# Optimization experiments

Measured on AMD Instinct MI355X. Metric: run time of the kernel, lower is better.

## Reference

```python
import math
import jax, jax.numpy as jnp
import numpy as np

B, L, D = 2, 2048, 1024
NH = 16
HS = D // NH
BLOCK_SIZE = 2048


def setup_inputs() -> dict:
    key = jax.random.key(0)
    ks = jax.random.split(key, 4)
    x = jax.random.normal(ks[0], (B, L, D), dtype=jnp.float32)
    Wqkv = jax.random.normal(ks[1], (D, 3 * D), dtype=jnp.float32) * 0.02
    bqkv = jnp.zeros((3 * D,), dtype=jnp.float32)
    Wproj = jax.random.normal(ks[2], (D, D), dtype=jnp.float32) * 0.02
    bproj = jnp.zeros((D,), dtype=jnp.float32)
    Er = jax.random.normal(ks[3], (BLOCK_SIZE, HS), dtype=jnp.float32)
    return {"x": x, "Wqkv": Wqkv, "bqkv": bqkv, "Wproj": Wproj, "bproj": bproj, "Er": Er}


def _skew(QEr):
    # QEr: [B, nh, L, L]  (Music Transformer skew trick)
    b, nh, nr, nc = QEr.shape
    padded = jnp.pad(QEr, ((0, 0), (0, 0), (0, 0), (1, 0)))  # [B, nh, nr, nc+1]
    reshaped = padded.reshape(b, nh, nc + 1, nr)
    return reshaped[:, :, 1:, :]  # [B, nh, nr, nc]


def reference(x, Wqkv, bqkv, Wproj, bproj, Er):
    b, l, d = x.shape
    qkv = x @ Wqkv + bqkv  # [B, L, 3D]
    q, k, v = jnp.split(qkv, 3, axis=2)
    q = q.reshape(b, l, NH, HS).transpose(0, 2, 1, 3)  # [B, nh, L, hs]
    k = k.reshape(b, l, NH, HS).transpose(0, 2, 1, 3)
    v = v.reshape(b, l, NH, HS).transpose(0, 2, 1, 3)

    start = BLOCK_SIZE - l
    Er_t = Er[start:, :].T  # [hs, L]
    QEr = jnp.einsum('bhld,dm->bhlm', q, Er_t)  # [B, nh, L, L]
    Srel = _skew(QEr)

    QK_t = jnp.einsum('bhld,bhmd->bhlm', q, k)
    scale = 1.0 / math.sqrt(HS)
    att = (QK_t + Srel) * scale
    causal = jnp.tril(jnp.ones((l, l), dtype=bool))
    att = jnp.where(causal[None, None, :, :], att, jnp.float32(-jnp.inf))
    att = jax.nn.softmax(att, axis=-1)
    y = jnp.einsum('bhlm,bhmd->bhld', att, v)
    y = y.transpose(0, 2, 1, 3).reshape(b, l, d)
    return y @ Wproj + bproj
```

## Files before the change

kernel.cpp:

```cpp
#include <hip/hip_runtime.h>
#include <stdint.h>

#define BB 2
#define LL 2048
#define DD 1024
#define NHH 16
#define HSS 64

typedef __bf16 bf16x8 __attribute__((ext_vector_type(8)));
typedef float f32x4 __attribute__((ext_vector_type(4)));

__device__ __forceinline__ bf16x8 load8(const float* p) {
  float4 f0 = *(const float4*)p;
  float4 f1 = *(const float4*)(p + 4);
  bf16x8 v;
  v[0] = (__bf16)f0.x; v[1] = (__bf16)f0.y; v[2] = (__bf16)f0.z; v[3] = (__bf16)f0.w;
  v[4] = (__bf16)f1.x; v[5] = (__bf16)f1.y; v[6] = (__bf16)f1.z; v[7] = (__bf16)f1.w;
  return v;
}
__device__ __forceinline__ bf16x8 load8(const __bf16* p) {
  return *(const bf16x8*)p;
}

__device__ __forceinline__ void async_ld16(__bf16* lds_uniform_base,
                                           const __bf16* gptr_per_lane) {
  __builtin_amdgcn_global_load_lds(
      (const __attribute__((address_space(1))) void*)gptr_per_lane,
      (__attribute__((address_space(3))) void*)lds_uniform_base, 16, 0, 0);
}

__global__ void prep_k(const float* __restrict__ Wqkv, const float* __restrict__ x,
                       const float* __restrict__ Er, __bf16* __restrict__ WqkvT,
                       __bf16* __restrict__ xb, __bf16* __restrict__ Erb) {
  int tx = threadIdx.x, ty = threadIdx.y;
  int tid = ty * 32 + tx;
  if (blockIdx.z == 1) {
    if (blockIdx.x >= 2048) return;
    size_t off = ((size_t)blockIdx.x * 256 + tid) * 8;
    *(bf16x8*)&xb[off] = load8(&x[off]);
    return;
  }
  if (blockIdx.z == 2) {
    if (blockIdx.x >= 64) return;
    size_t off = ((size_t)blockIdx.x * 256 + tid) * 8;
    *(bf16x8*)&Erb[off] = load8(&Er[off]);
    return;
  }
  __shared__ __bf16 tile[32][33];
  int c0 = (blockIdx.x % 96) * 32, r0 = (blockIdx.x / 96) * 32;
#pragma unroll
  for (int i = ty; i < 32; i += 8)
    tile[i][tx] = (__bf16)Wqkv[(size_t)(r0 + i) * 3072 + c0 + tx];
  __syncthreads();
#pragma unroll
  for (int i = ty; i < 32; i += 8)
    WqkvT[(size_t)(c0 + i) * 1024 + r0 + tx] = tile[tx][i];
}

__global__ void tconv_k(const float* __restrict__ src, __bf16* __restrict__ dst,
                        int R, int C) {
  __shared__ __bf16 tile[32][33];
  int c0 = blockIdx.x * 32, r0 = blockIdx.y * 32;
  int tx = threadIdx.x, ty = threadIdx.y;
#pragma unroll
  for (int i = ty; i < 32; i += 8)
    tile[i][tx] = (__bf16)src[(size_t)(r0 + i) * C + c0 + tx];
  __syncthreads();
#pragma unroll
  for (int i = ty; i < 32; i += 8)
    dst[(size_t)(c0 + i) * R + r0 + tx] = tile[tx][i];
}

__global__ __launch_bounds__(256) void gemm_qkv_k(
    const __bf16* __restrict__ A, const __bf16* __restrict__ Bt,
    const float* __restrict__ bias, __bf16* __restrict__ Qo,
    __bf16* __restrict__ Ko, __bf16* __restrict__ Vto) {
  const int K = 1024;
  __shared__ __align__(16) __bf16 As[128 * 32];
  __shared__ __align__(16) __bf16 Bs[128 * 32];
  int t = threadIdx.x;
  int wave = t >> 6, lane = t & 63, qd = lane >> 4, lr = lane & 15;
  int m0 = blockIdx.y * 128, n0 = blockIdx.x * 128;
  int wm = (wave >> 1) * 64, wn = (wave & 1) * 64;
  f32x4 acc[4][4] = {};
  int srow = lane >> 2, sch = (lane & 3) * 8;
  const __bf16* Ab[2];
  const __bf16* Bb[2];
#pragma unroll
  for (int c = 0; c < 2; c++) {
    Ab[c] = A + (size_t)(m0 + (wave * 2 + c) * 16 + srow) * K + sch;
    Bb[c] = Bt + (size_t)(n0 + (wave * 2 + c) * 16 + srow) * K + sch;
  }
  for (int k0 = 0; k0 < K; k0 += 32) {
    __syncthreads();
#pragma unroll
    for (int c = 0; c < 2; c++) {
      async_ld16(&As[(wave * 2 + c) * 512], Ab[c] + k0);
      async_ld16(&Bs[(wave * 2 + c) * 512], Bb[c] + k0);
    }
    __syncthreads();
    bf16x8 af[4], bfr[4];
#pragma unroll
    for (int mt = 0; mt < 4; mt++)
      af[mt] = *(const bf16x8*)&As[(wm + mt * 16 + lr) * 32 + qd * 8];
#pragma unroll
    for (int nt = 0; nt < 4; nt++)
      bfr[nt] = *(const bf16x8*)&Bs[(wn + nt * 16 + lr) * 32 + qd * 8];
#pragma unroll
    for (int mt = 0; mt < 4; mt++)
#pragma unroll
      for (int nt = 0; nt < 4; nt++)
        acc[mt][nt] = __builtin_amdgcn_mfma_f32_16x16x32_bf16(af[mt], bfr[nt],
                                                              acc[mt][nt], 0, 0, 0);
  }
  float bvv[4];
#pragma unroll
  for (int nt = 0; nt < 4; nt++) bvv[nt] = bias[n0 + wn + nt * 16 + lr];
#pragma unroll
  for (int mt = 0; mt < 4; mt++)
#pragma unroll
    for (int nt = 0; nt < 4; nt++)
#pragma unroll
      for (int r = 0; r < 4; r++) {
        int row = m0 + wm + mt * 16 + qd * 4 + r;
        int col = n0 + wn + nt * 16 + lr;
        __bf16 bb = (__bf16)(acc[mt][nt][r] + bvv[nt]);
        int b = row >> 11, l = row & 2047;
        int h = (col >> 6) & 15, d = col & 63;
        if (col < DD) {
          Qo[(((size_t)(b * NHH + h)) * LL + l) * HSS + d] = bb;
        } else if (col < 2 * DD) {
          Ko[(((size_t)(b * NHH + h)) * LL + l) * HSS + d] = bb;
        } else {
          Vto[(((size_t)(b * NHH + h)) * HSS + d) * LL + l] = bb;
        }
      }
}

__global__ __launch_bounds__(256) void gemm_proj_k(
    const __bf16* __restrict__ A, const __bf16* __restrict__ Bt,
    const float* __restrict__ bias, float* __restrict__ out) {
  const int K = 1024, N = 1024;
  __shared__ __align__(16) __bf16 As[128 * 32];
  __shared__ __align__(16) __bf16 Bs[64 * 32];
  int t = threadIdx.x;
  int wave = t >> 6, lane = t & 63, qd = lane >> 4, lr = lane & 15;
  int m0 = blockIdx.y * 128, n0 = blockIdx.x * 64;
  int wm = (wave >> 1) * 64, wn = (wave & 1) * 32;
  f32x4 acc[4][2] = {};
  int srow = lane >> 2, sch = (lane & 3) * 8;
  const __bf16* Ab[2];
  const __bf16* Bb;
#pragma unroll
  for (int c = 0; c < 2; c++)
    Ab[c] = A + (size_t)(m0 + (wave * 2 + c) * 16 + srow) * K + sch;
  Bb = Bt + (size_t)(n0 + wave * 16 + srow) * K + sch;

  for (int k0 = 0; k0 < K; k0 += 32) {
    __syncthreads();
#pragma unroll
    for (int c = 0; c < 2; c++)
      async_ld16(&As[(wave * 2 + c) * 512], Ab[c] + k0);
    async_ld16(&Bs[wave * 512], Bb + k0);
    __syncthreads();
    bf16x8 af[4], bfr[2];
#pragma unroll
    for (int mt = 0; mt < 4; mt++)
      af[mt] = *(const bf16x8*)&As[(wm + mt * 16 + lr) * 32 + qd * 8];
#pragma unroll
    for (int nt = 0; nt < 2; nt++)
      bfr[nt] = *(const bf16x8*)&Bs[(wn + nt * 16 + lr) * 32 + qd * 8];
#pragma unroll
    for (int mt = 0; mt < 4; mt++)
#pragma unroll
      for (int nt = 0; nt < 2; nt++)
        acc[mt][nt] = __builtin_amdgcn_mfma_f32_16x16x32_bf16(af[mt], bfr[nt],
                                                              acc[mt][nt], 0, 0, 0);
  }
  float bvv[2];
#pragma unroll
  for (int nt = 0; nt < 2; nt++) bvv[nt] = bias[n0 + wn + nt * 16 + lr];
#pragma unroll
  for (int mt = 0; mt < 4; mt++)
#pragma unroll
    for (int nt = 0; nt < 2; nt++)
#pragma unroll
      for (int r = 0; r < 4; r++) {
        int row = m0 + wm + mt * 16 + qd * 4 + r;
        int col = n0 + wn + nt * 16 + lr;
        out[(size_t)row * N + col] = acc[mt][nt][r] + bvv[nt];
      }
}

__global__ __launch_bounds__(256, 4) void flash_k(
    const __bf16* __restrict__ Qg, const __bf16* __restrict__ Kg,
    const __bf16* __restrict__ Vtg, const __bf16* __restrict__ Erb,
    __bf16* __restrict__ Yg) {
  __shared__ __align__(16) __bf16 Kld[64 * 72];
  __shared__ __align__(16) __bf16 Vld[64 * 72];
  __shared__ __align__(16) __bf16 Pball[4][16 * 72];

  int bh = blockIdx.x;
  int i0 = (31 - (int)blockIdx.y) * 64;
  const __bf16* Qh = Qg + (size_t)bh * LL * HSS;
  const __bf16* Kh = Kg + (size_t)bh * LL * HSS;
  const __bf16* Vth = Vtg + (size_t)bh * HSS * LL;
  int b = bh >> 4, h = bh & 15;
  int t = threadIdx.x, wave = t >> 6, lane = t & 63, qd = lane >> 4, lr = lane & 15;
  __bf16* Pb = &Pball[wave][0];
  int cbase = 48 - wave * 16;

  bf16x8 bones;
#pragma unroll
  for (int q = 0; q < 8; q++) bones[q] = (lr == 0) ? (__bf16)1.f : (__bf16)0.f;

  int jj = t >> 2, hf = t & 3;

  bf16x8 aq[2];
  {
    const __bf16* qrow = Qh + (size_t)(i0 + wave * 16 + lr) * HSS + qd * 8;
    aq[0] = *(const bf16x8*)qrow;
    aq[1] = *(const bf16x8*)(qrow + 32);
  }
  f32x4 oacc[5] = {};

  bf16x8 kr0, kr1, vr0, vr1;
  auto prefetch = [&](int j0) {
    kr0 = *(const bf16x8*)&Kh[(size_t)(j0 + jj) * HSS + hf * 16];
    kr1 = *(const bf16x8*)&Kh[(size_t)(j0 + jj) * HSS + hf * 16 + 8];
    vr0 = *(const bf16x8*)&Vth[(size_t)jj * LL + j0 + hf * 16];
    vr1 = *(const bf16x8*)&Vth[(size_t)jj * LL + j0 + hf * 16 + 8];
  };
  prefetch(0);

  for (int j0 = 0; j0 <= i0; j0 += 64) {
    __syncthreads();
    *(bf16x8*)&Kld[jj * 72 + hf * 16] = kr0;
    *(bf16x8*)&Kld[jj * 72 + hf * 16 + 8] = kr1;
    *(bf16x8*)&Vld[jj * 72 + hf * 16] = vr0;
    *(bf16x8*)&Vld[jj * 72 + hf * 16 + 8] = vr1;
    __syncthreads();
    if (j0 + 64 <= i0) prefetch(j0 + 64);

    bf16x8 ef[5][2];
    int ebase = LL - 64 - i0 + j0 + cbase;
#pragma unroll
    for (int ct = 0; ct < 5; ct++) {
      int e = ebase + ct * 16 + lr;
      e = (e < LL) ? e : (LL - 1);
#pragma unroll
      for (int kc = 0; kc < 2; kc++)
        ef[ct][kc] = *(const bf16x8*)&Erb[(size_t)e * HSS + kc * 32 + qd * 8];
    }

    f32x4 sacc[4] = {};
#pragma unroll
    for (int ct = 0; ct < 4; ct++)
#pragma unroll
      for (int kc = 0; kc < 2; kc++) {
        bf16x8 bk = *(const bf16x8*)&Kld[(ct * 16 + lr) * 72 + kc * 32 + qd * 8];
        sacc[ct] = __builtin_amdgcn_mfma_f32_16x16x32_bf16(aq[kc], bk, sacc[ct], 0, 0, 0);
      }
    f32x4 racc[5] = {};
#pragma unroll
    for (int ct = 0; ct < 5; ct++)
#pragma unroll
      for (int kc = 0; kc < 2; kc++)
        racc[ct] = __builtin_amdgcn_mfma_f32_16x16x32_bf16(aq[kc], ef[ct][kc],
                                                           racc[ct], 0, 0, 0);

#pragma unroll
    for (int r = 0; r < 4; r++) {
      int tr = qd * 4 + r;
      int base = 15 - tr + lr;
      int src = qd * 16 + (base & 15);
      int hi = base >> 4;
      float sh[5];
#pragma unroll
      for (int ct = 0; ct < 5; ct++) sh[ct] = __shfl(racc[ct][r], src, 64);
      int gi = i0 + wave * 16 + tr;
#pragma unroll
      for (int ct2 = 0; ct2 < 4; ct2++) {
        float rel = hi ? sh[ct2 + 1] : sh[ct2];
        float s = (sacc[ct2][r] + rel) * 0.125f;
        int gj = j0 + ct2 * 16 + lr;
        float p = (gj <= gi) ? __expf(s) : 0.f;
        Pb[tr * 72 + ct2 * 16 + lr] = (__bf16)p;
      }
    }

    bf16x8 ap0 = *(const bf16x8*)&Pb[lr * 72 + qd * 8];
    bf16x8 ap1 = *(const bf16x8*)&Pb[lr * 72 + 32 + qd * 8];
#pragma unroll
    for (int dt = 0; dt < 4; dt++) {
      bf16x8 bv0 = *(const bf16x8*)&Vld[(dt * 16 + lr) * 72 + qd * 8];
      bf16x8 bv1 = *(const bf16x8*)&Vld[(dt * 16 + lr) * 72 + 32 + qd * 8];
      oacc[dt] = __builtin_amdgcn_mfma_f32_16x16x32_bf16(ap0, bv0, oacc[dt], 0, 0, 0);
      oacc[dt] = __builtin_amdgcn_mfma_f32_16x16x32_bf16(ap1, bv1, oacc[dt], 0, 0, 0);
    }
    oacc[4] = __builtin_amdgcn_mfma_f32_16x16x32_bf16(ap0, bones, oacc[4], 0, 0, 0);
    oacc[4] = __builtin_amdgcn_mfma_f32_16x16x32_bf16(ap1, bones, oacc[4], 0, 0, 0);
  }

#pragma unroll
  for (int r = 0; r < 4; r++) {
    float lv = __shfl(oacc[4][r], qd * 16, 64);
    float inv = 1.f / lv;
    int l = i0 + wave * 16 + qd * 4 + r;
#pragma unroll
    for (int dt = 0; dt < 4; dt++) {
      int d = dt * 16 + lr;
      Yg[((size_t)(b * LL) + l) * DD + h * HSS + d] = (__bf16)(oacc[dt][r] * inv);
    }
  }
}

extern "C" void kernel_launch(void* const* d_in, const int* in_sizes, int n_in,
                              void* d_out, int out_size, void* d_ws, size_t ws_size,
                              hipStream_t stream) {
  const float* x = (const float*)d_in[0];
  const float* Wqkv = (const float*)d_in[1];
  const float* bqkv = (const float*)d_in[2];
  const float* Wproj = (const float*)d_in[3];
  const float* bproj = (const float*)d_in[4];
  const float* Er = (const float*)d_in[5];
  float* out = (float*)d_out;

  if (ws_size < 4u * 8388608u) return;

  uint8_t* w = (uint8_t*)d_ws;
  __bf16* Q = (__bf16*)w;  w += (size_t)BB * NHH * LL * HSS * 2;
  __bf16* Kt = (__bf16*)w; w += (size_t)BB * NHH * LL * HSS * 2;
  __bf16* Vt = (__bf16*)w; w += (size_t)BB * NHH * LL * HSS * 2;
  __bf16* Y = (__bf16*)w;  w += (size_t)BB * LL * DD * 2;

  __bf16* WqkvT = (__bf16*)d_out;
  __bf16* xb = (__bf16*)((uint8_t*)d_out + (size_t)3072 * 1024 * 2);
  __bf16* Erb = (__bf16*)((uint8_t*)d_out + (size_t)3072 * 1024 * 2 + (size_t)4096 * 1024 * 2);
  __bf16* WprojT = Q;

  prep_k<<<dim3(3072, 1, 3), dim3(32, 8), 0, stream>>>(Wqkv, x, Er, WqkvT, xb, Erb);
  gemm_qkv_k<<<dim3(3072 / 128, 4096 / 128), 256, 0, stream>>>(
      xb, WqkvT, bqkv, Q, Kt, Vt);
  flash_k<<<dim3(BB * NHH, 32), 256, 0, stream>>>(Q, Kt, Vt, Erb, Y);
  tconv_k<<<dim3(1024 / 32, 1024 / 32), dim3(32, 8), 0, stream>>>(Wproj, WprojT, 1024, 1024);
  gemm_proj_k<<<dim3(1024 / 64, 4096 / 128), 256, 0, stream>>>(Y, WprojT, bproj, out);
}
```

Before: 265.7 us.

## Split causal flash attention KV range in two and add combine kernel

Each query tile's key/value loop is split into two halves handled by separate blocks (grid z=2). Each block writes an unnormalized bf16 partial output and its row-sum to scratch, and a new combine kernel adds the two halves and normalizes. The aim is more parallel blocks and a shorter critical path for the long causal tiles. The cost is an extra kernel launch, extra global traffic, and bf16 rounding of the partials. Launch bounds also drop from 4 to 3 blocks per CU.

Measured after the change: 251.0 us (median of 2 runs). 5.5% less time.

```diff
diff --git a/kernel.cpp b/kernel.cpp
--- a/kernel.cpp
+++ b/kernel.cpp
@@ -192,16 +192,22 @@
       }
 }
 
-__global__ __launch_bounds__(256, 4) void flash_k(
+__global__ __launch_bounds__(256, 3) void flash_k(
     const __bf16* __restrict__ Qg, const __bf16* __restrict__ Kg,
     const __bf16* __restrict__ Vtg, const __bf16* __restrict__ Erb,
-    __bf16* __restrict__ Yg) {
+    __bf16* __restrict__ Po0, __bf16* __restrict__ Po1,
+    float* __restrict__ Lp0, float* __restrict__ Lp1) {
   __shared__ __align__(16) __bf16 Kld[64 * 72];
   __shared__ __align__(16) __bf16 Vld[64 * 72];
   __shared__ __align__(16) __bf16 Pball[4][16 * 72];
 
   int bh = blockIdx.x;
-  int i0 = (31 - (int)blockIdx.y) * 64;
+  int tile = 31 - (int)blockIdx.y;
+  int i0 = tile * 64;
+  int niter = tile + 1;
+  int mid = (niter + 1) >> 1;
+  int it0 = (blockIdx.z == 0) ? 0 : mid;
+  int it1 = (blockIdx.z == 0) ? mid : niter;
   const __bf16* Qh = Qg + (size_t)bh * LL * HSS;
   const __bf16* Kh = Kg + (size_t)bh * LL * HSS;
   const __bf16* Vth = Vtg + (size_t)bh * HSS * LL;
@@ -231,16 +237,17 @@
     vr0 = *(const bf16x8*)&Vth[(size_t)jj * LL + j0 + hf * 16];
     vr1 = *(const bf16x8*)&Vth[(size_t)jj * LL + j0 + hf * 16 + 8];
   };
-  prefetch(0);
-
-  for (int j0 = 0; j0 <= i0; j0 += 64) {
+  if (it0 < it1) prefetch(it0 * 64);
+
+  for (int it = it0; it < it1; ++it) {
+    int j0 = it * 64;
     __syncthreads();
     *(bf16x8*)&Kld[jj * 72 + hf * 16] = kr0;
     *(bf16x8*)&Kld[jj * 72 + hf * 16 + 8] = kr1;
     *(bf16x8*)&Vld[jj * 72 + hf * 16] = vr0;
     *(bf16x8*)&Vld[jj * 72 + hf * 16 + 8] = vr1;
     __syncthreads();
-    if (j0 + 64 <= i0) prefetch(j0 + 64);
+    if (it + 1 < it1) prefetch((it + 1) * 64);
 
     bf16x8 ef[5][2];
     int ebase = LL - 64 - i0 + j0 + cbase;
@@ -302,17 +309,39 @@
     oacc[4] = __builtin_amdgcn_mfma_f32_16x16x32_bf16(ap1, bones, oacc[4], 0, 0, 0);
   }
 
+  __bf16* Po = (blockIdx.z == 0) ? Po0 : Po1;
+  float* Lp = (blockIdx.z == 0) ? Lp0 : Lp1;
 #pragma unroll
   for (int r = 0; r < 4; r++) {
-    float lv = __shfl(oacc[4][r], qd * 16, 64);
-    float inv = 1.f / lv;
     int l = i0 + wave * 16 + qd * 4 + r;
+    if (lr == 0) Lp[(size_t)bh * LL + l] = oacc[4][r];
 #pragma unroll
     for (int dt = 0; dt < 4; dt++) {
       int d = dt * 16 + lr;
-      Yg[((size_t)(b * LL) + l) * DD + h * HSS + d] = (__bf16)(oacc[dt][r] * inv);
-    }
-  }
+      Po[((size_t)(b * LL) + l) * DD + h * HSS + d] = (__bf16)oacc[dt][r];
+    }
+  }
+}
+
+__global__ void combine_k(const __bf16* __restrict__ Po0,
+                          const __bf16* __restrict__ Po1,
+                          const float* __restrict__ Lp0,
+                          const float* __restrict__ Lp1,
+                          __bf16* __restrict__ Y) {
+  size_t f = ((size_t)blockIdx.x * 256 + threadIdx.x) * 8;
+  int dfull = (int)(f & 1023);
+  int h = dfull >> 6;
+  int l = (int)((f >> 10) & 2047);
+  int b = (int)(f >> 21);
+  size_t lidx = ((size_t)(b * NHH + h)) * LL + l;
+  float linv = 1.f / (Lp0[lidx] + Lp1[lidx]);
+  bf16x8 a = *(const bf16x8*)&Po0[f];
+  bf16x8 c = *(const bf16x8*)&Po1[f];
+  bf16x8 o;
+#pragma unroll
+  for (int q = 0; q < 8; q++)
+    o[q] = (__bf16)(((float)a[q] + (float)c[q]) * linv);
+  *(bf16x8*)&Y[f] = o;
 }
 
 extern "C" void kernel_launch(void* const* d_in, const int* in_sizes, int n_in,
@@ -337,12 +366,18 @@
   __bf16* WqkvT = (__bf16*)d_out;
   __bf16* xb = (__bf16*)((uint8_t*)d_out + (size_t)3072 * 1024 * 2);
   __bf16* Erb = (__bf16*)((uint8_t*)d_out + (size_t)3072 * 1024 * 2 + (size_t)4096 * 1024 * 2);
+  __bf16* Po1 = (__bf16*)d_out;
+  float* Lp0 = (float*)((uint8_t*)d_out + (size_t)BB * LL * DD * 2);
+  float* Lp1 = (float*)((uint8_t*)d_out + (size_t)BB * LL * DD * 2 + (size_t)BB * NHH * LL * 4);
+  __bf16* Po0 = Y;
   __bf16* WprojT = Q;
 
   prep_k<<<dim3(3072, 1, 3), dim3(32, 8), 0, stream>>>(Wqkv, x, Er, WqkvT, xb, Erb);
   gemm_qkv_k<<<dim3(3072 / 128, 4096 / 128), 256, 0, stream>>>(
       xb, WqkvT, bqkv, Q, Kt, Vt);
-  flash_k<<<dim3(BB * NHH, 32), 256, 0, stream>>>(Q, Kt, Vt, Erb, Y);
+  flash_k<<<dim3(BB * NHH, 32, 2), 256, 0, stream>>>(
+      Q, Kt, Vt, Erb, Po0, Po1, Lp0, Lp1);
+  combine_k<<<dim3(2048), 256, 0, stream>>>(Po0, Po1, Lp0, Lp1, Y);
   tconv_k<<<dim3(1024 / 32, 1024 / 32), dim3(32, 8), 0, stream>>>(Wproj, WprojT, 1024, 1024);
   gemm_proj_k<<<dim3(1024 / 64, 4096 / 128), 256, 0, stream>>>(Y, WprojT, bproj, out);
 }
```

## Use single-wave flash blocks with register-resident K/V fragments instead of shared memory

Applied to the files above, without the earlier changes.

The attention kernel now launches one 64-thread wave per 16-row query tile instead of four waves sharing a 64-row tile. K and V fragments are loaded straight from global memory into registers, with a software prefetch of the next tile, so the shared-memory staging and both __syncthreads per iteration go away. The causal loop length is now computed per 16-row tile, which trims some masked work. In exchange K/V are no longer shared between waves, so global/L2 traffic for K and V rises up to fourfold and register pressure grows.

New measurement: 359.8 us. 1.35x slower.

```diff
diff --git a/kernel.cpp b/kernel.cpp
--- a/kernel.cpp
+++ b/kernel.cpp
@@ -192,75 +192,80 @@
       }
 }
 
-__global__ __launch_bounds__(256, 4) void flash_k(
+__global__ __launch_bounds__(64, 3) void flash_k(
     const __bf16* __restrict__ Qg, const __bf16* __restrict__ Kg,
     const __bf16* __restrict__ Vtg, const __bf16* __restrict__ Erb,
     __bf16* __restrict__ Yg) {
-  __shared__ __align__(16) __bf16 Kld[64 * 72];
-  __shared__ __align__(16) __bf16 Vld[64 * 72];
-  __shared__ __align__(16) __bf16 Pball[4][16 * 72];
+  __shared__ __align__(16) __bf16 Pb[16 * 72];
 
   int bh = blockIdx.x;
-  int i0 = (31 - (int)blockIdx.y) * 64;
+  int tile = 127 - (int)blockIdx.y;
+  int i0 = tile * 16;
+  int niter = (i0 >> 6) + 1;
   const __bf16* Qh = Qg + (size_t)bh * LL * HSS;
   const __bf16* Kh = Kg + (size_t)bh * LL * HSS;
   const __bf16* Vth = Vtg + (size_t)bh * HSS * LL;
   int b = bh >> 4, h = bh & 15;
-  int t = threadIdx.x, wave = t >> 6, lane = t & 63, qd = lane >> 4, lr = lane & 15;
-  __bf16* Pb = &Pball[wave][0];
-  int cbase = 48 - wave * 16;
+  int lane = threadIdx.x & 63, qd = lane >> 4, lr = lane & 15;
 
   bf16x8 bones;
 #pragma unroll
   for (int q = 0; q < 8; q++) bones[q] = (lr == 0) ? (__bf16)1.f : (__bf16)0.f;
-
-  int jj = t >> 2, hf = t & 3;
 
   bf16x8 aq[2];
   {
-    const __bf16* qrow = Qh + (size_t)(i0 + wave * 16 + lr) * HSS + qd * 8;
+    const __bf16* qrow = Qh + (size_t)(i0 + lr) * HSS + qd * 8;
     aq[0] = *(const bf16x8*)qrow;
     aq[1] = *(const bf16x8*)(qrow + 32);
   }
   f32x4 oacc[5] = {};
 
-  bf16x8 kr0, kr1, vr0, vr1;
-  auto prefetch = [&](int j0) {
-    kr0 = *(const bf16x8*)&Kh[(size_t)(j0 + jj) * HSS + hf * 16];
-    kr1 = *(const bf16x8*)&Kh[(size_t)(j0 + jj) * HSS + hf * 16 + 8];
-    vr0 = *(const bf16x8*)&Vth[(size_t)jj * LL + j0 + hf * 16];
-    vr1 = *(const bf16x8*)&Vth[(size_t)jj * LL + j0 + hf * 16 + 8];
+  bf16x8 kf[4][2], vf[4][2], ef[5][2];
+  auto loadK = [&](int j0) {
+#pragma unroll
+    for (int ct = 0; ct < 4; ct++) {
+      const __bf16* kr = Kh + (size_t)(j0 + ct * 16 + lr) * HSS + qd * 8;
+#pragma unroll
+      for (int kc = 0; kc < 2; kc++) kf[ct][kc] = *(const bf16x8*)(kr + kc * 32);
+    }
   };
-  prefetch(0);
-
-  for (int j0 = 0; j0 <= i0; j0 += 64) {
-    __syncthreads();
-    *(bf16x8*)&Kld[jj * 72 + hf * 16] = kr0;
-    *(bf16x8*)&Kld[jj * 72 + hf * 16 + 8] = kr1;
-    *(bf16x8*)&Vld[jj * 72 + hf * 16] = vr0;
-    *(bf16x8*)&Vld[jj * 72 + hf * 16 + 8] = vr1;
-    __syncthreads();
-    if (j0 + 64 <= i0) prefetch(j0 + 64);
-
-    bf16x8 ef[5][2];
-    int ebase = LL - 64 - i0 + j0 + cbase;
+  auto loadV = [&](int j0) {
+#pragma unroll
+    for (int dt = 0; dt < 4; dt++) {
+      const __bf16* vr = Vth + (size_t)(dt * 16 + lr) * LL + j0 + qd * 8;
+#pragma unroll
+      for (int kc = 0; kc < 2; kc++) vf[dt][kc] = *(const bf16x8*)(vr + kc * 32);
+    }
+  };
+  auto loadE = [&](int j0) {
+    int ebase = LL - 16 - i0 + j0;
 #pragma unroll
     for (int ct = 0; ct < 5; ct++) {
       int e = ebase + ct * 16 + lr;
       e = (e < LL) ? e : (LL - 1);
+      const __bf16* er = Erb + (size_t)e * HSS + qd * 8;
+#pragma unroll
+      for (int kc = 0; kc < 2; kc++) ef[ct][kc] = *(const bf16x8*)(er + kc * 32);
+    }
+  };
+
+  loadK(0);
+  loadV(0);
+
+  for (int it = 0; it < niter; ++it) {
+    int j0 = it * 64;
+    bool more = (it + 1 < niter);
+    loadE(j0);
+
+    f32x4 sacc[4] = {};
+#pragma unroll
+    for (int ct = 0; ct < 4; ct++)
 #pragma unroll
       for (int kc = 0; kc < 2; kc++)
-        ef[ct][kc] = *(const bf16x8*)&Erb[(size_t)e * HSS + kc * 32 + qd * 8];
-    }
-
-    f32x4 sacc[4] = {};
-#pragma unroll
-    for (int ct = 0; ct < 4; ct++)
-#pragma unroll
-      for (int kc = 0; kc < 2; kc++) {
-        bf16x8 bk = *(const bf16x8*)&Kld[(ct * 16 + lr) * 72 + kc * 32 + qd * 8];
-        sacc[ct] = __builtin_amdgcn_mfma_f32_16x16x32_bf16(aq[kc], bk, sacc[ct], 0, 0, 0);
-      }
+        sacc[ct] = __builtin_amdgcn_mfma_f32_16x16x32_bf16(aq[kc], kf[ct][kc],
+                                                           sacc[ct], 0, 0, 0);
+    if (more) loadK(j0 + 64);
+
     f32x4 racc[5] = {};
 #pragma unroll
     for (int ct = 0; ct < 5; ct++)
@@ -278,7 +283,7 @@
       float sh[5];
 #pragma unroll
       for (int ct = 0; ct < 5; ct++) sh[ct] = __shfl(racc[ct][r], src, 64);
-      int gi = i0 + wave * 16 + tr;
+      int gi = i0 + tr;
 #pragma unroll
       for (int ct2 = 0; ct2 < 4; ct2++) {
         float rel = hi ? sh[ct2 + 1] : sh[ct2];
@@ -293,20 +298,19 @@
     bf16x8 ap1 = *(const bf16x8*)&Pb[lr * 72 + 32 + qd * 8];
 #pragma unroll
     for (int dt = 0; dt < 4; dt++) {
-      bf16x8 bv0 = *(const bf16x8*)&Vld[(dt * 16 + lr) * 72 + qd * 8];
-      bf16x8 bv1 = *(const bf16x8*)&Vld[(dt * 16 + lr) * 72 + 32 + qd * 8];
-      oacc[dt] = __builtin_amdgcn_mfma_f32_16x16x32_bf16(ap0, bv0, oacc[dt], 0, 0, 0);
-      oacc[dt] = __builtin_amdgcn_mfma_f32_16x16x32_bf16(ap1, bv1, oacc[dt], 0, 0, 0);
+      oacc[dt] = __builtin_amdgcn_mfma_f32_16x16x32_bf16(ap0, vf[dt][0], oacc[dt], 0, 0, 0);
+      oacc[dt] = __builtin_amdgcn_mfma_f32_16x16x32_bf16(ap1, vf[dt][1], oacc[dt], 0, 0, 0);
     }
     oacc[4] = __builtin_amdgcn_mfma_f32_16x16x32_bf16(ap0, bones, oacc[4], 0, 0, 0);
     oacc[4] = __builtin_amdgcn_mfma_f32_16x16x32_bf16(ap1, bones, oacc[4], 0, 0, 0);
+    if (more) loadV(j0 + 64);
   }
 
 #pragma unroll
   for (int r = 0; r < 4; r++) {
     float lv = __shfl(oacc[4][r], qd * 16, 64);
     float inv = 1.f / lv;
-    int l = i0 + wave * 16 + qd * 4 + r;
+    int l = i0 + qd * 4 + r;
 #pragma unroll
     for (int dt = 0; dt < 4; dt++) {
       int d = dt * 16 + lr;
@@ -342,7 +346,7 @@
   prep_k<<<dim3(3072, 1, 3), dim3(32, 8), 0, stream>>>(Wqkv, x, Er, WqkvT, xb, Erb);
   gemm_qkv_k<<<dim3(3072 / 128, 4096 / 128), 256, 0, stream>>>(
       xb, WqkvT, bqkv, Q, Kt, Vt);
-  flash_k<<<dim3(BB * NHH, 32), 256, 0, stream>>>(Q, Kt, Vt, Erb, Y);
+  flash_k<<<dim3(BB * NHH, 128), 64, 0, stream>>>(Q, Kt, Vt, Erb, Y);
   tconv_k<<<dim3(1024 / 32, 1024 / 32), dim3(32, 8), 0, stream>>>(Wproj, WprojT, 1024, 1024);
   gemm_proj_k<<<dim3(1024 / 64, 4096 / 128), 256, 0, stream>>>(Y, WprojT, bproj, out);
 }
```
